# Kernel optimization log

Hardware: AMD Instinct MI355X
Metric: run time of the kernel (lower is better)

The kernel has to match this reference:

```python
import jax, jax.numpy as jnp
import numpy as np

ALPHA = 0.2  # LeakyReLU negative slope

def setup_inputs() -> dict:
    key = jax.random.key(0)
    k1, k2, k3, k4 = jax.random.split(key, 4)
    N, F_in, F_out = 8192, 512, 64
    x = jax.random.normal(k1, (N, F_in), dtype=jnp.float32)
    adj = jax.random.randint(k2, (N, N), 0, 2, dtype=jnp.int32)
    # xavier-normal-ish init
    weight = jax.random.normal(k3, (F_in, F_out), dtype=jnp.float32) * np.sqrt(2.0 / (F_in + F_out))
    a = jax.random.normal(k4, (2 * F_out, 1), dtype=jnp.float32) * np.sqrt(2.0 / (2 * F_out + 1))
    return {"x": x, "adj": adj, "weight": weight, "a": a}

def reference(x, adj, weight, a):
    # Wh: [N, F_out]
    Wh = x @ weight
    F_out = weight.shape[1]
    a1 = a[:F_out, 0]   # applies to source (row) node
    a2 = a[F_out:, 0]   # applies to target (col) node
    # e[i,j] = LeakyReLU(Wh[i]@a1 + Wh[j]@a2)  -- broadcast-add instead of O(N^2*2F) concat
    s1 = Wh @ a1        # [N]
    s2 = Wh @ a2        # [N]
    e = s1[:, None] + s2[None, :]              # [N, N]
    e = jnp.where(e > 0, e, ALPHA * e)         # LeakyReLU
    e = jnp.where(adj > 0, e, jnp.float32(-9e15))
    attention = jax.nn.softmax(e, axis=1)      # [N, N]
    h_prime = attention @ Wh                   # [N, F_out]
    return jax.nn.elu(h_prime)                 # concat=True -> ELU
```

## Files before the change

### kernel.cpp

```cpp
#include <hip/hip_runtime.h>
#include <hip/hip_bf16.h>
#include <cstdint>
#include <cstddef>

#define N_NODES 8192
#define F_IN 512
#define F_OUT 64
#define LOG2E 1.44269504f

#define JSPLIT 4
#define JPB (N_NODES / JSPLIT)
#define JC 256
#define NCHUNK (JPB / JC)

typedef __attribute__((ext_vector_type(8))) short short8v;
typedef __attribute__((ext_vector_type(4))) float f32x4;
typedef __attribute__((ext_vector_type(4))) int i32x4;
typedef __attribute__((ext_vector_type(4))) unsigned int u32x4;

static __device__ __forceinline__ unsigned short f2bf(float f) {
    union { float f; unsigned u; } v; v.f = f;
    unsigned u = v.u + 0x7FFFu + ((v.u >> 16) & 1u);
    return (unsigned short)(u >> 16);
}
static __device__ __forceinline__ float bf2f(unsigned short b) {
    union { unsigned u; float f; } v; v.u = ((unsigned)b) << 16;
    return v.f;
}
static __device__ __forceinline__ unsigned cvt_pk_bf16(float lo, float hi) {
    unsigned r;
    asm("v_cvt_pk_bf16_f32 %0, %1, %2" : "=v"(r) : "v"(lo), "v"(hi));
    return r;
}

__global__ __launch_bounds__(256)
void gat_wconv(const float* __restrict__ W, unsigned short* __restrict__ whf,
               unsigned short* __restrict__ wlf) {
    const int t = blockIdx.x * 256 + threadIdx.x;
    const int tile = t >> 6, lane = t & 63;
    const int kt = tile >> 2, ct = tile & 3;
    const int k0 = kt * 32 + ((lane >> 4) << 3);
    const int c  = ct * 16 + (lane & 15);
    short8v h, l;
    #pragma unroll
    for (int i = 0; i < 8; ++i) {
        float v = W[(size_t)(k0 + i) * F_OUT + c];
        unsigned short hb = f2bf(v);
        h[i] = (short)hb;
        l[i] = (short)f2bf(v - bf2f(hb));
    }
    const size_t dst = (size_t)tile * 512 + (size_t)lane * 8;
    *(short8v*)(whf + dst) = h;
    *(short8v*)(wlf + dst) = l;
}

__global__ __launch_bounds__(128)
void gat_prep(const float* __restrict__ x, const unsigned short* __restrict__ whf,
              const unsigned short* __restrict__ wlf, const float* __restrict__ a,
              unsigned short* __restrict__ whtf,
              float* __restrict__ s1, float* __restrict__ s2) {
    __shared__ unsigned short ldsT[64][40];
    const int tid = threadIdx.x;
    const int lane = tid & 63;
    const int wv = tid >> 6;
    const int l15 = lane & 15, g = lane >> 4;
    const int jt = blockIdx.x;
    const int row0 = jt * 32 + wv * 16;

    f32x4 acc[4] = {{0.f,0.f,0.f,0.f},{0.f,0.f,0.f,0.f},{0.f,0.f,0.f,0.f},{0.f,0.f,0.f,0.f}};

    const float4* xp = (const float4*)(x + (size_t)(row0 + l15) * F_IN) + g * 2;
    for (int kb = 0; kb < 4; ++kb) {
        float4 v[8];
        #pragma unroll
        for (int q = 0; q < 4; ++q) {
            v[2 * q]     = xp[q * 8];
            v[2 * q + 1] = xp[q * 8 + 1];
        }
        xp += 32;
        #pragma unroll
        for (int q = 0; q < 4; ++q) {
            const int kt = kb * 4 + q;
            float vv[8] = {v[2*q].x, v[2*q].y, v[2*q].z, v[2*q].w,
                           v[2*q+1].x, v[2*q+1].y, v[2*q+1].z, v[2*q+1].w};
            short8v xh, xl;
            #pragma unroll
            for (int i = 0; i < 8; ++i) {
                unsigned short hb = f2bf(vv[i]);
                xh[i] = (short)hb;
                xl[i] = (short)f2bf(vv[i] - bf2f(hb));
            }
            const unsigned short* wp = whf + (size_t)(kt * 4) * 512 + (size_t)lane * 8;
            const unsigned short* lp = wlf + (size_t)(kt * 4) * 512 + (size_t)lane * 8;
            #pragma unroll
            for (int ct = 0; ct < 4; ++ct) {
                short8v wh = *(const short8v*)(wp + ct * 512);
                short8v wl = *(const short8v*)(lp + ct * 512);
                acc[ct] = __builtin_amdgcn_mfma_f32_16x16x32_bf16(xh, wh, acc[ct], 0, 0, 0);
                acc[ct] = __builtin_amdgcn_mfma_f32_16x16x32_bf16(xl, wh, acc[ct], 0, 0, 0);
                acc[ct] = __builtin_amdgcn_mfma_f32_16x16x32_bf16(xh, wl, acc[ct], 0, 0, 0);
            }
        }
    }

    #pragma unroll
    for (int r = 0; r < 4; ++r) {
        float p1 = 0.f, p2 = 0.f;
        #pragma unroll
        for (int ct = 0; ct < 4; ++ct) {
            p1 = fmaf(acc[ct][r], a[ct * 16 + l15], p1);
            p2 = fmaf(acc[ct][r], a[64 + ct * 16 + l15], p2);
        }
        p1 += __shfl_xor(p1, 1); p2 += __shfl_xor(p2, 1);
        p1 += __shfl_xor(p1, 2); p2 += __shfl_xor(p2, 2);
        p1 += __shfl_xor(p1, 4); p2 += __shfl_xor(p2, 4);
        p1 += __shfl_xor(p1, 8); p2 += __shfl_xor(p2, 8);
        if (l15 == 0) {
            s1[row0 + g * 4 + r] = p1 * LOG2E;
            s2[row0 + g * 4 + r] = p2 * LOG2E;
        }
    }

    #pragma unroll
    for (int ct = 0; ct < 4; ++ct) {
        ushort4 pk;
        pk.x = f2bf(acc[ct][0]); pk.y = f2bf(acc[ct][1]);
        pk.z = f2bf(acc[ct][2]); pk.w = f2bf(acc[ct][3]);
        *(ushort4*)&ldsT[ct * 16 + l15][wv * 16 + g * 4] = pk;
    }
    __syncthreads();

    #pragma unroll
    for (int fl = 0; fl < 2; ++fl) {
        const int ft = wv * 2 + fl;
        short8v sv = *(const short8v*)&ldsT[ft * 16 + l15][g * 8];
        *(short8v*)(whtf + ((size_t)jt * 4 + ft) * 512 + (size_t)lane * 8) = sv;
    }
}

__global__ __launch_bounds__(512)
void gat_main(const int* __restrict__ adj, const unsigned short* __restrict__ whtf,
              const float* __restrict__ s1, const float* __restrict__ s2,
              float* __restrict__ numpart, float* __restrict__ denpart) {
    __shared__ unsigned short lds[2][JC * F_OUT];
    const int tid  = threadIdx.x;
    const int lane = tid & 63;
    const int wv   = tid >> 6;
    const int l15  = lane & 15, g = lane >> 4;
    const int rg   = blockIdx.x >> 2;
    const int js   = blockIdx.x & 3;
    const int rowbase = rg * 128 + wv * 16;
    const int row  = rowbase + l15;
    const int j0   = js * JPB;
    const float s1r = s1[row];

    const char* gbase = (const char*)whtf + (size_t)j0 * 128;
    const int*   aprow = adj + (size_t)row * N_NODES + j0 + g * 8;
    const float* s2b   = s2 + j0 + g * 8;

    f32x4 acc0 = {0.f, 0.f, 0.f, 0.f};
    f32x4 acc1 = acc0, acc2 = acc0, acc3 = acc0;
    float dsum = 0.f;

    #define STAGE(ch, buf) do { \
        const char* _g = gbase + (size_t)(ch) * 32768 + (size_t)tid * 16; \
        char* _l = (char*)&lds[buf][0] + (size_t)wv * 1024; \
        _Pragma("unroll") \
        for (int _i = 0; _i < 4; ++_i) \
            __builtin_amdgcn_global_load_lds( \
                (const __attribute__((address_space(1))) void*)(_g + _i * 8192), \
                (__attribute__((address_space(3))) void*)(_l + _i * 8192), 16, 0, 0); \
    } while (0)

    STAGE(0, 0);
    __syncthreads();

    for (int ch = 0; ch < NCHUNK; ++ch) {
        const int cur = ch & 1;
        if (ch < NCHUNK - 1) STAGE(ch + 1, cur ^ 1);

        const unsigned short* lbuf = &lds[cur][0];
        #pragma unroll 2
        for (int it = 0; it < 8; ++it) {
            const int jw = ch * JC + it * 32;
            const i32x4* ap = (const i32x4*)(aprow + jw);
            i32x4  aj0 = ap[0];
            i32x4  aj1 = ap[1];
            float4 sa  = *(const float4*)(s2b + jw);
            float4 sb  = *(const float4*)(s2b + jw + 4);

            short8v b0 = *(const short8v*)(lbuf + (it * 4 + 0) * 512 + lane * 8);
            short8v b1 = *(const short8v*)(lbuf + (it * 4 + 1) * 512 + lane * 8);
            short8v b2 = *(const short8v*)(lbuf + (it * 4 + 2) * 512 + lane * 8);
            short8v b3 = *(const short8v*)(lbuf + (it * 4 + 3) * 512 + lane * 8);

            float w0, w1, w2, w3, w4, w5, w6, w7;
            #define GAT_EL(wvar, ajv, s2v) do { \
                float e = s1r + (s2v); e = fmaxf(e, 0.2f * e); \
                float ex = __builtin_amdgcn_exp2f(e); \
                wvar = ((ajv) > 0) ? ex : 0.f; dsum += wvar; } while (0);
            GAT_EL(w0, aj0[0], sa.x) GAT_EL(w1, aj0[1], sa.y)
            GAT_EL(w2, aj0[2], sa.z) GAT_EL(w3, aj0[3], sa.w)
            GAT_EL(w4, aj1[0], sb.x) GAT_EL(w5, aj1[1], sb.y)
            GAT_EL(w6, aj1[2], sb.z) GAT_EL(w7, aj1[3], sb.w)
            #undef GAT_EL

            u32x4 au;
            au[0] = cvt_pk_bf16(w0, w1);
            au[1] = cvt_pk_bf16(w2, w3);
            au[2] = cvt_pk_bf16(w4, w5);
            au[3] = cvt_pk_bf16(w6, w7);
            short8v afrag = __builtin_bit_cast(short8v, au);

            acc0 = __builtin_amdgcn_mfma_f32_16x16x32_bf16(afrag, b0, acc0, 0, 0, 0);
            acc1 = __builtin_amdgcn_mfma_f32_16x16x32_bf16(afrag, b1, acc1, 0, 0, 0);
            acc2 = __builtin_amdgcn_mfma_f32_16x16x32_bf16(afrag, b2, acc2, 0, 0, 0);
            acc3 = __builtin_amdgcn_mfma_f32_16x16x32_bf16(afrag, b3, acc3, 0, 0, 0);
        }
        __syncthreads();
    }
    #undef STAGE

    dsum += __shfl_xor(dsum, 16);
    dsum += __shfl_xor(dsum, 32);
    if (lane < 16) denpart[(size_t)js * N_NODES + rowbase + lane] = dsum;

    float* np = numpart + ((size_t)js * N_NODES + rowbase) * F_OUT;
    #pragma unroll
    for (int r = 0; r < 4; ++r) {
        const int ro = (g * 4 + r) * F_OUT;
        np[ro +  0 + l15] = acc0[r];
        np[ro + 16 + l15] = acc1[r];
        np[ro + 32 + l15] = acc2[r];
        np[ro + 48 + l15] = acc3[r];
    }
}

__global__ __launch_bounds__(256)
void gat_combine(const float* __restrict__ numpart, const float* __restrict__ denpart,
                 float* __restrict__ out) {
    const int idx = blockIdx.x * 256 + threadIdx.x;
    const int r = idx >> 6;
    float num = 0.f, den = 0.f;
    #pragma unroll
    for (int c = 0; c < JSPLIT; ++c) {
        num += numpart[(size_t)c * N_NODES * F_OUT + idx];
        den += denpart[(size_t)c * N_NODES + r];
    }
    float h = num / den;
    out[idx] = h > 0.f ? h : __expf(h) - 1.f;
}

extern "C" void kernel_launch(void* const* d_in, const int* in_sizes, int n_in,
                              void* d_out, int out_size, void* d_ws, size_t ws_size,
                              hipStream_t stream) {
    const float* x      = (const float*)d_in[0];
    const int*   adj    = (const int*)d_in[1];
    const float* weight = (const float*)d_in[2];
    const float* a      = (const float*)d_in[3];
    float* out = (float*)d_out;

    char* ws = (char*)d_ws;
    unsigned short* whtf = (unsigned short*)ws;
    float* s1            = (float*)(ws + 1048576);
    float* s2            = (float*)(ws + 1048576 + 32768);
    unsigned short* whf  = (unsigned short*)(ws + 1048576 + 65536);
    unsigned short* wlf  = (unsigned short*)(ws + 1048576 + 131072);
    float* numpart       = (float*)(ws + 1048576 + 196608);
    float* denpart       = (float*)(ws + 1048576 + 196608 + 8388608);

    gat_wconv<<<16, 256, 0, stream>>>(weight, whf, wlf);
    gat_prep<<<N_NODES / 32, 128, 0, stream>>>(x, whf, wlf, a, whtf, s1, s2);
    gat_main<<<64 * JSPLIT, 512, 0, stream>>>(adj, whtf, s1, s2, numpart, denpart);
    gat_combine<<<N_NODES * F_OUT / 256, 256, 0, stream>>>(numpart, denpart, out);
}
```

Baseline: 89.32 us.

## Double j-split, split prep GEMM over K, and batch adjacency loads

Increases the column split of the attention kernel from 4 to 8 so more blocks run concurrently, and batches adjacency loads for four inner iterations to raise memory-level parallelism. The prep kernel now uses 256 threads, splitting K between wave pairs and reducing the partial sums through LDS. The cost is double the partial numerator/denominator traffic in the combine step, plus extra register pressure from the batched loads.

New measurement: 85.97 us (median of 2 runs). 1.04x faster.

```diff
diff --git a/kernel.cpp b/kernel.cpp
--- a/kernel.cpp
+++ b/kernel.cpp
@@ -8,7 +8,7 @@
 #define F_OUT 64
 #define LOG2E 1.44269504f
 
-#define JSPLIT 4
+#define JSPLIT 8
 #define JPB (N_NODES / JSPLIT)
 #define JC 256
 #define NCHUNK (JPB / JC)
@@ -54,87 +54,100 @@
     *(short8v*)(wlf + dst) = l;
 }
 
-__global__ __launch_bounds__(128)
+__global__ __launch_bounds__(256)
 void gat_prep(const float* __restrict__ x, const unsigned short* __restrict__ whf,
               const unsigned short* __restrict__ wlf, const float* __restrict__ a,
               unsigned short* __restrict__ whtf,
               float* __restrict__ s1, float* __restrict__ s2) {
+    __shared__ f32x4 red[2][4][64];
     __shared__ unsigned short ldsT[64][40];
     const int tid = threadIdx.x;
     const int lane = tid & 63;
     const int wv = tid >> 6;
+    const int rt = wv & 1;
+    const int kh = wv >> 1;
     const int l15 = lane & 15, g = lane >> 4;
     const int jt = blockIdx.x;
-    const int row0 = jt * 32 + wv * 16;
+    const int row0 = jt * 32 + rt * 16;
 
     f32x4 acc[4] = {{0.f,0.f,0.f,0.f},{0.f,0.f,0.f,0.f},{0.f,0.f,0.f,0.f},{0.f,0.f,0.f,0.f}};
 
-    const float4* xp = (const float4*)(x + (size_t)(row0 + l15) * F_IN) + g * 2;
-    for (int kb = 0; kb < 4; ++kb) {
-        float4 v[8];
-        #pragma unroll
-        for (int q = 0; q < 4; ++q) {
-            v[2 * q]     = xp[q * 8];
-            v[2 * q + 1] = xp[q * 8 + 1];
-        }
-        xp += 32;
-        #pragma unroll
-        for (int q = 0; q < 4; ++q) {
-            const int kt = kb * 4 + q;
-            float vv[8] = {v[2*q].x, v[2*q].y, v[2*q].z, v[2*q].w,
-                           v[2*q+1].x, v[2*q+1].y, v[2*q+1].z, v[2*q+1].w};
-            short8v xh, xl;
-            #pragma unroll
-            for (int i = 0; i < 8; ++i) {
-                unsigned short hb = f2bf(vv[i]);
-                xh[i] = (short)hb;
-                xl[i] = (short)f2bf(vv[i] - bf2f(hb));
-            }
-            const unsigned short* wp = whf + (size_t)(kt * 4) * 512 + (size_t)lane * 8;
-            const unsigned short* lp = wlf + (size_t)(kt * 4) * 512 + (size_t)lane * 8;
+    const float* xp = x + (size_t)(row0 + l15) * F_IN + kh * 256 + g * 8;
+    float4 v[16];
+    #pragma unroll
+    for (int q = 0; q < 8; ++q) {
+        v[2 * q]     = *(const float4*)(xp + q * 32);
+        v[2 * q + 1] = *(const float4*)(xp + q * 32 + 4);
+    }
+    #pragma unroll
+    for (int q = 0; q < 8; ++q) {
+        const int kt = kh * 8 + q;
+        float vv[8] = {v[2*q].x, v[2*q].y, v[2*q].z, v[2*q].w,
+                       v[2*q+1].x, v[2*q+1].y, v[2*q+1].z, v[2*q+1].w};
+        short8v xh, xl;
+        #pragma unroll
+        for (int i = 0; i < 8; ++i) {
+            unsigned short hb = f2bf(vv[i]);
+            xh[i] = (short)hb;
+            xl[i] = (short)f2bf(vv[i] - bf2f(hb));
+        }
+        const unsigned short* wp = whf + (size_t)(kt * 4) * 512 + (size_t)lane * 8;
+        const unsigned short* lp = wlf + (size_t)(kt * 4) * 512 + (size_t)lane * 8;
+        #pragma unroll
+        for (int ct = 0; ct < 4; ++ct) {
+            short8v wh = *(const short8v*)(wp + ct * 512);
+            short8v wl = *(const short8v*)(lp + ct * 512);
+            acc[ct] = __builtin_amdgcn_mfma_f32_16x16x32_bf16(xh, wh, acc[ct], 0, 0, 0);
+            acc[ct] = __builtin_amdgcn_mfma_f32_16x16x32_bf16(xl, wh, acc[ct], 0, 0, 0);
+            acc[ct] = __builtin_amdgcn_mfma_f32_16x16x32_bf16(xh, wl, acc[ct], 0, 0, 0);
+        }
+    }
+
+    if (kh == 1) {
+        #pragma unroll
+        for (int ct = 0; ct < 4; ++ct) red[rt][ct][lane] = acc[ct];
+    }
+    __syncthreads();
+
+    if (kh == 0) {
+        #pragma unroll
+        for (int ct = 0; ct < 4; ++ct) acc[ct] += red[rt][ct][lane];
+
+        #pragma unroll
+        for (int r = 0; r < 4; ++r) {
+            float p1 = 0.f, p2 = 0.f;
             #pragma unroll
             for (int ct = 0; ct < 4; ++ct) {
-                short8v wh = *(const short8v*)(wp + ct * 512);
-                short8v wl = *(const short8v*)(lp + ct * 512);
-                acc[ct] = __builtin_amdgcn_mfma_f32_16x16x32_bf16(xh, wh, acc[ct], 0, 0, 0);
-                acc[ct] = __builtin_amdgcn_mfma_f32_16x16x32_bf16(xl, wh, acc[ct], 0, 0, 0);
-                acc[ct] = __builtin_amdgcn_mfma_f32_16x16x32_bf16(xh, wl, acc[ct], 0, 0, 0);
-            }
-        }
-    }
-
-    #pragma unroll
-    for (int r = 0; r < 4; ++r) {
-        float p1 = 0.f, p2 = 0.f;
+                p1 = fmaf(acc[ct][r], a[ct * 16 + l15], p1);
+                p2 = fmaf(acc[ct][r], a[64 + ct * 16 + l15], p2);
+            }
+            p1 += __shfl_xor(p1, 1); p2 += __shfl_xor(p2, 1);
+            p1 += __shfl_xor(p1, 2); p2 += __shfl_xor(p2, 2);
+            p1 += __shfl_xor(p1, 4); p2 += __shfl_xor(p2, 4);
+            p1 += __shfl_xor(p1, 8); p2 += __shfl_xor(p2, 8);
+            if (l15 == 0) {
+                s1[row0 + g * 4 + r] = p1 * LOG2E;
+                s2[row0 + g * 4 + r] = p2 * LOG2E;
+            }
+        }
+
         #pragma unroll
         for (int ct = 0; ct < 4; ++ct) {
-            p1 = fmaf(acc[ct][r], a[ct * 16 + l15], p1);
-            p2 = fmaf(acc[ct][r], a[64 + ct * 16 + l15], p2);
-        }
-        p1 += __shfl_xor(p1, 1); p2 += __shfl_xor(p2, 1);
-        p1 += __shfl_xor(p1, 2); p2 += __shfl_xor(p2, 2);
-        p1 += __shfl_xor(p1, 4); p2 += __shfl_xor(p2, 4);
-        p1 += __shfl_xor(p1, 8); p2 += __shfl_xor(p2, 8);
-        if (l15 == 0) {
-            s1[row0 + g * 4 + r] = p1 * LOG2E;
-            s2[row0 + g * 4 + r] = p2 * LOG2E;
-        }
-    }
-
-    #pragma unroll
-    for (int ct = 0; ct < 4; ++ct) {
-        ushort4 pk;
-        pk.x = f2bf(acc[ct][0]); pk.y = f2bf(acc[ct][1]);
-        pk.z = f2bf(acc[ct][2]); pk.w = f2bf(acc[ct][3]);
-        *(ushort4*)&ldsT[ct * 16 + l15][wv * 16 + g * 4] = pk;
+            ushort4 pk;
+            pk.x = f2bf(acc[ct][0]); pk.y = f2bf(acc[ct][1]);
+            pk.z = f2bf(acc[ct][2]); pk.w = f2bf(acc[ct][3]);
+            *(ushort4*)&ldsT[ct * 16 + l15][rt * 16 + g * 4] = pk;
+        }
     }
     __syncthreads();
 
-    #pragma unroll
-    for (int fl = 0; fl < 2; ++fl) {
-        const int ft = wv * 2 + fl;
-        short8v sv = *(const short8v*)&ldsT[ft * 16 + l15][g * 8];
-        *(short8v*)(whtf + ((size_t)jt * 4 + ft) * 512 + (size_t)lane * 8) = sv;
+    if (kh == 0) {
+        #pragma unroll
+        for (int fl = 0; fl < 2; ++fl) {
+            const int ft = rt * 2 + fl;
+            short8v sv = *(const short8v*)&ldsT[ft * 16 + l15][g * 8];
+            *(short8v*)(whtf + ((size_t)jt * 4 + ft) * 512 + (size_t)lane * 8) = sv;
+        }
     }
 }
 
@@ -147,8 +160,8 @@
     const int lane = tid & 63;
     const int wv   = tid >> 6;
     const int l15  = lane & 15, g = lane >> 4;
-    const int rg   = blockIdx.x >> 2;
-    const int js   = blockIdx.x & 3;
+    const int rg   = blockIdx.x >> 3;
+    const int js   = blockIdx.x & 7;
     const int rowbase = rg * 128 + wv * 16;
     const int row  = rowbase + l15;
     const int j0   = js * JPB;
@@ -180,42 +193,50 @@
         if (ch < NCHUNK - 1) STAGE(ch + 1, cur ^ 1);
 
         const unsigned short* lbuf = &lds[cur][0];
-        #pragma unroll 2
-        for (int it = 0; it < 8; ++it) {
-            const int jw = ch * JC + it * 32;
-            const i32x4* ap = (const i32x4*)(aprow + jw);
-            i32x4  aj0 = ap[0];
-            i32x4  aj1 = ap[1];
-            float4 sa  = *(const float4*)(s2b + jw);
-            float4 sb  = *(const float4*)(s2b + jw + 4);
-
-            short8v b0 = *(const short8v*)(lbuf + (it * 4 + 0) * 512 + lane * 8);
-            short8v b1 = *(const short8v*)(lbuf + (it * 4 + 1) * 512 + lane * 8);
-            short8v b2 = *(const short8v*)(lbuf + (it * 4 + 2) * 512 + lane * 8);
-            short8v b3 = *(const short8v*)(lbuf + (it * 4 + 3) * 512 + lane * 8);
-
-            float w0, w1, w2, w3, w4, w5, w6, w7;
-            #define GAT_EL(wvar, ajv, s2v) do { \
-                float e = s1r + (s2v); e = fmaxf(e, 0.2f * e); \
-                float ex = __builtin_amdgcn_exp2f(e); \
-                wvar = ((ajv) > 0) ? ex : 0.f; dsum += wvar; } while (0);
-            GAT_EL(w0, aj0[0], sa.x) GAT_EL(w1, aj0[1], sa.y)
-            GAT_EL(w2, aj0[2], sa.z) GAT_EL(w3, aj0[3], sa.w)
-            GAT_EL(w4, aj1[0], sb.x) GAT_EL(w5, aj1[1], sb.y)
-            GAT_EL(w6, aj1[2], sb.z) GAT_EL(w7, aj1[3], sb.w)
-            #undef GAT_EL
-
-            u32x4 au;
-            au[0] = cvt_pk_bf16(w0, w1);
-            au[1] = cvt_pk_bf16(w2, w3);
-            au[2] = cvt_pk_bf16(w4, w5);
-            au[3] = cvt_pk_bf16(w6, w7);
-            short8v afrag = __builtin_bit_cast(short8v, au);
-
-            acc0 = __builtin_amdgcn_mfma_f32_16x16x32_bf16(afrag, b0, acc0, 0, 0, 0);
-            acc1 = __builtin_amdgcn_mfma_f32_16x16x32_bf16(afrag, b1, acc1, 0, 0, 0);
-            acc2 = __builtin_amdgcn_mfma_f32_16x16x32_bf16(afrag, b2, acc2, 0, 0, 0);
-            acc3 = __builtin_amdgcn_mfma_f32_16x16x32_bf16(afrag, b3, acc3, 0, 0, 0);
+        #pragma unroll
+        for (int itg = 0; itg < 2; ++itg) {
+            i32x4 aj[8];
+            #pragma unroll
+            for (int q = 0; q < 4; ++q) {
+                const i32x4* ap = (const i32x4*)(aprow + ch * JC + itg * 128 + q * 32);
+                aj[2 * q]     = ap[0];
+                aj[2 * q + 1] = ap[1];
+            }
+            #pragma unroll
+            for (int q = 0; q < 4; ++q) {
+                const int it = itg * 4 + q;
+                const int jw = ch * JC + it * 32;
+                float4 sa = *(const float4*)(s2b + jw);
+                float4 sb = *(const float4*)(s2b + jw + 4);
+
+                short8v b0 = *(const short8v*)(lbuf + (it * 4 + 0) * 512 + lane * 8);
+                short8v b1 = *(const short8v*)(lbuf + (it * 4 + 1) * 512 + lane * 8);
+                short8v b2 = *(const short8v*)(lbuf + (it * 4 + 2) * 512 + lane * 8);
+                short8v b3 = *(const short8v*)(lbuf + (it * 4 + 3) * 512 + lane * 8);
+
+                float w0, w1, w2, w3, w4, w5, w6, w7;
+                #define GAT_EL(wvar, ajv, s2v) do { \
+                    float e = s1r + (s2v); e = fmaxf(e, 0.2f * e); \
+                    float ex = __builtin_amdgcn_exp2f(e); \
+                    wvar = ((ajv) > 0) ? ex : 0.f; dsum += wvar; } while (0);
+                GAT_EL(w0, aj[2*q][0], sa.x) GAT_EL(w1, aj[2*q][1], sa.y)
+                GAT_EL(w2, aj[2*q][2], sa.z) GAT_EL(w3, aj[2*q][3], sa.w)
+                GAT_EL(w4, aj[2*q+1][0], sb.x) GAT_EL(w5, aj[2*q+1][1], sb.y)
+                GAT_EL(w6, aj[2*q+1][2], sb.z) GAT_EL(w7, aj[2*q+1][3], sb.w)
+                #undef GAT_EL
+
+                u32x4 au;
+                au[0] = cvt_pk_bf16(w0, w1);
+                au[1] = cvt_pk_bf16(w2, w3);
+                au[2] = cvt_pk_bf16(w4, w5);
+                au[3] = cvt_pk_bf16(w6, w7);
+                short8v afrag = __builtin_bit_cast(short8v, au);
+
+                acc0 = __builtin_amdgcn_mfma_f32_16x16x32_bf16(afrag, b0, acc0, 0, 0, 0);
+                acc1 = __builtin_amdgcn_mfma_f32_16x16x32_bf16(afrag, b1, acc1, 0, 0, 0);
+                acc2 = __builtin_amdgcn_mfma_f32_16x16x32_bf16(afrag, b2, acc2, 0, 0, 0);
+                acc3 = __builtin_amdgcn_mfma_f32_16x16x32_bf16(afrag, b3, acc3, 0, 0, 0);
+            }
         }
         __syncthreads();
     }
@@ -267,10 +288,10 @@
     unsigned short* whf  = (unsigned short*)(ws + 1048576 + 65536);
     unsigned short* wlf  = (unsigned short*)(ws + 1048576 + 131072);
     float* numpart       = (float*)(ws + 1048576 + 196608);
-    float* denpart       = (float*)(ws + 1048576 + 196608 + 8388608);
+    float* denpart       = (float*)(ws + 1048576 + 196608 + (size_t)JSPLIT * N_NODES * F_OUT * 4);
 
     gat_wconv<<<16, 256, 0, stream>>>(weight, whf, wlf);
-    gat_prep<<<N_NODES / 32, 128, 0, stream>>>(x, whf, wlf, a, whtf, s1, s2);
+    gat_prep<<<N_NODES / 32, 256, 0, stream>>>(x, whf, wlf, a, whtf, s1, s2);
     gat_main<<<64 * JSPLIT, 512, 0, stream>>>(adj, whtf, s1, s2, numpart, denpart);
     gat_combine<<<N_NODES * F_OUT / 256, 256, 0, stream>>>(numpart, denpart, out);
 }
```
